# Performance work log

Measured on AMD Instinct MI355X. Metric: run time of the kernel, lower is better.

The kernel has to match this reference:

```python
import jax, jax.numpy as jnp
import numpy as np
from jax import lax

B, H, W, C, NH = 16, 56, 56, 192, 6
L = H * W
DH = C // NH            # 32
HID = 4 * C             # 768
ETA = 1.0 / DH          # TTT inner-loop learning rate
EPS = 1e-5

# ---- RoPE rotation tables (deterministic buffer, shape (H, W, C//2)) ----
_kmax = C // 4
_theta = 1.0 / (10000.0 ** (np.arange(_kmax) / _kmax))
_ii, _jj = np.meshgrid(np.arange(H), np.arange(W), indexing='ij')
_ang = np.concatenate([_ii[..., None] * _theta, _jj[..., None] * _theta], axis=-1)  # (H,W,C/2)
_COS = jnp.asarray(np.cos(_ang), dtype=jnp.float32)
_SIN = jnp.asarray(np.sin(_ang), dtype=jnp.float32)


def layernorm(x, g, b):
    mu = jnp.mean(x, axis=-1, keepdims=True)
    var = jnp.mean(jnp.square(x - mu), axis=-1, keepdims=True)
    return (x - mu) * lax.rsqrt(var + EPS) * g + b


def dwconv3x3(x_blc, w, b):
    # x: (B, L, Ch) -> depthwise 3x3 conv over (H, W) -> (B, L, Ch)
    Ch = x_blc.shape[-1]
    xi = x_blc.reshape(B, H, W, Ch).transpose(0, 3, 1, 2)  # NCHW
    y = lax.conv_general_dilated(xi, w, (1, 1), 'SAME', feature_group_count=Ch,
                                 dimension_numbers=('NCHW', 'OIHW', 'NCHW'))
    y = y + b[None, :, None, None]
    return y.transpose(0, 2, 3, 1).reshape(B, L, Ch)


def rope(x):
    # x: (B, L, C); rotate complex pairs with 2D axial angles
    xr = x.reshape(B, H, W, C // 2, 2)
    re, im = xr[..., 0], xr[..., 1]
    o_re = _COS * re - _SIN * im
    o_im = _SIN * re + _COS * im
    return jnp.stack([o_re, o_im], axis=-1).reshape(B, L, C)


def ttt_attn(xn, qkv_w, qkv_b, W0, proj_w, proj_b):
    qkv = xn @ qkv_w.T + qkv_b                      # (B, L, 3C)
    q, k, v = jnp.split(qkv, 3, axis=-1)
    q = rope(q) * (DH ** -0.5)
    k = rope(k)

    def to_heads(t):  # (B,L,C) -> (L, B*NH, DH)
        return t.reshape(B, L, NH, DH).transpose(1, 0, 2, 3).reshape(L, B * NH, DH)
    qs, ks, vs = to_heads(q), to_heads(k), to_heads(v)

    Wst0 = jnp.broadcast_to(W0[None], (B, NH, DH, DH)).reshape(B * NH, DH, DH)

    def step(Wst, qkv_t):
        qt, kt, vt = qkv_t
        pred = jnp.einsum('bij,bj->bi', Wst, kt)
        Wn = Wst - ETA * (pred - vt)[:, :, None] * kt[:, None, :]
        ot = jnp.einsum('bij,bj->bi', Wn, qt)
        return Wn, ot

    _, out = lax.scan(step, Wst0, (qs, ks, vs))     # out: (L, B*NH, DH)
    out = out.reshape(L, B, NH, DH).transpose(1, 0, 2, 3).reshape(B, L, C)
    return out @ proj_w.T + proj_b


def setup_inputs() -> dict:
    key = jax.random.key(0)
    ks = jax.random.split(key, 12)
    s = 0.02
    return {
        'x': jax.random.normal(ks[0], (B, L, C), jnp.float32),
        'cpe_w': jax.random.normal(ks[1], (C, 1, 3, 3), jnp.float32) * s,
        'cpe_b': jnp.zeros((C,), jnp.float32),
        'n1_g': jnp.ones((C,), jnp.float32),
        'n1_b': jnp.zeros((C,), jnp.float32),
        'qkv_w': jax.random.normal(ks[2], (3 * C, C), jnp.float32) * s,
        'qkv_b': jnp.zeros((3 * C,), jnp.float32),
        'W0': jax.random.normal(ks[3], (NH, DH, DH), jnp.float32) * s,
        'proj_w': jax.random.normal(ks[4], (C, C), jnp.float32) * s,
        'proj_b': jnp.zeros((C,), jnp.float32),
        'n2_g': jnp.ones((C,), jnp.float32),
        'n2_b': jnp.zeros((C,), jnp.float32),
        'fc1_w': jax.random.normal(ks[5], (HID, C), jnp.float32) * s,
        'fc1_b': jnp.zeros((HID,), jnp.float32),
        'dwc_w': jax.random.normal(ks[6], (HID, 1, 3, 3), jnp.float32) * s,
        'dwc_b': jnp.zeros((HID,), jnp.float32),
        'fc2_w': jax.random.normal(ks[7], (C, HID), jnp.float32) * s,
        'fc2_b': jnp.zeros((C,), jnp.float32),
    }


def reference(x, cpe_w, cpe_b, n1_g, n1_b, qkv_w, qkv_b, W0, proj_w, proj_b,
              n2_g, n2_b, fc1_w, fc1_b, dwc_w, dwc_b, fc2_w, fc2_b):
    # CPE: conditional positional encoding (depthwise conv residual)
    x = x + dwconv3x3(x, cpe_w, cpe_b)
    # TTT attention branch
    x = x + ttt_attn(layernorm(x, n1_g, n1_b), qkv_w, qkv_b, W0, proj_w, proj_b)
    # MLP branch with depthwise conv
    h1 = jax.nn.gelu(layernorm(x, n2_g, n2_b) @ fc1_w.T + fc1_b, approximate=False)
    h1 = jax.nn.gelu(h1 + dwconv3x3(h1, dwc_w, dwc_b), approximate=False)
    x = x + (h1 @ fc2_w.T + fc2_b)
    return x
```

## Files before the change

kernel.cpp:

```cpp
#include <hip/hip_runtime.h>
#include <hip/hip_bf16.h>

#define Bc 16
#define Hc 56
#define Wcc 56
#define Cc 192
#define NHc 6
#define Lc 3136
#define DHc 32
#define HIDc 768
#define NHEAD 96
#define Sc 32
#define NCHUNK 98
#define NPAIR (NHEAD*NCHUNK)
#define ROWS (Bc*Lc)
#define GR2 (ROWS/2)
#define ETAc (1.0f/32.0f)

typedef unsigned short u16;
typedef unsigned int u32;
typedef __attribute__((ext_vector_type(8))) short bf16x8;
typedef __attribute__((ext_vector_type(4))) float f32x4;
typedef __attribute__((ext_vector_type(16))) float f32x16;

__device__ __forceinline__ float b2f(u16 v){ u32 u = ((u32)v)<<16; float f; __builtin_memcpy(&f,&u,4); return f; }
__device__ __forceinline__ u16 f2b(float f){ u32 u; __builtin_memcpy(&u,&f,4); u32 r = u + 0x7FFFu + ((u>>16)&1u); return (u16)(r>>16); }
__device__ __forceinline__ f32x16 zero16(){ f32x16 z = {0,0,0,0,0,0,0,0,0,0,0,0,0,0,0,0}; return z; }

__device__ __forceinline__ void make_bfrags(const f32x16& t, int hi, bf16x8& b1, bf16x8& b2){
  u32 P[8], S[8];
  #pragma unroll
  for (int q=0;q<4;q++){
    #pragma unroll
    for (int j=0;j<2;j++){
      u32 r; float lo = t[4*q+2*j], hv = t[4*q+2*j+1];
      asm("v_cvt_pk_bf16_f32 %0, %1, %2" : "=v"(r) : "v"(lo), "v"(hv));
      P[2*q+j] = r;
    }
  }
  #pragma unroll
  for (int i=0;i<8;i++) S[i] = (u32)__shfl_xor((int)P[i], 32);
  union { u32 u[4]; bf16x8 v; } f1, f2;
  if (hi==0){ f1.u[0]=P[0]; f1.u[1]=P[1]; f1.u[2]=S[0]; f1.u[3]=S[1];
              f2.u[0]=P[4]; f2.u[1]=P[5]; f2.u[2]=S[4]; f2.u[3]=S[5]; }
  else      { f1.u[0]=S[2]; f1.u[1]=S[3]; f1.u[2]=P[2]; f1.u[3]=P[3];
              f2.u[0]=S[6]; f2.u[1]=S[7]; f2.u[2]=P[6]; f2.u[3]=P[7]; }
  b1 = f1.v; b2 = f2.v;
}

__global__ __launch_bounds__(256) void prep_kernel(
    const float* __restrict__ qkvw, const float* __restrict__ projw,
    const float* __restrict__ fc1w, const float* __restrict__ fc2w,
    const float* __restrict__ dwcw, const float* __restrict__ cpew,
    u16* __restrict__ wbqkv, u16* __restrict__ wbproj, u16* __restrict__ wbfc1,
    u16* __restrict__ wbfc2, float* __restrict__ dwt9, float* __restrict__ cwt9){
  int i = blockIdx.x*256 + threadIdx.x;
  if (i < 110592) wbqkv[i] = f2b(qkvw[i]);
  else if (i < 147456){ int j=i-110592; wbproj[j] = f2b(projw[j]); }
  else if (i < 294912){ int j=i-147456; wbfc1[j] = f2b(fc1w[j]); }
  else if (i < 442368){ int j=i-294912; wbfc2[j] = f2b(fc2w[j]); }
  else if (i < 449280){ int j=i-442368; int ch=j/9, t=j-ch*9; dwt9[t*HIDc+ch] = dwcw[j]; }
  else if (i < 451008){ int j=i-449280; int ch=j/9, t=j-ch*9; cwt9[t*Cc+ch] = cpew[j]; }
}

__global__ __launch_bounds__(256) void rope_tab_kernel(float* __restrict__ ct, float* __restrict__ st){
  int i = blockIdx.x*256 + threadIdx.x;
  int l = i/96, p = i - l*96;
  int h = l/Wcc, w = l - h*Wcc;
  int kk = (p<48)? p : p-48;
  float th = powf(10000.f, -(float)kk/48.f);
  float ang = (float)((p<48)? h : w) * th;
  ct[i] = cosf(ang);
  st[i] = sinf(ang);
}

__global__ __launch_bounds__(192) void cpe_ln_kernel(const float* __restrict__ x, const float* __restrict__ cwt9,
                                                     const float* __restrict__ bs, const float* __restrict__ g,
                                                     const float* __restrict__ b,
                                                     u16* __restrict__ x1, u16* __restrict__ xn){
  __shared__ float ps[192], pq[192], smu[8], srs[8];
  int tid = threadIdx.x;
  int rl = tid/24, sub = tid - rl*24, ch0 = sub*8;
  int row = blockIdx.x*8 + rl;
  int l = row % Lc; int h = l/Wcc, w = l - h*Wcc;
  const float* xp = x + (size_t)row*Cc + ch0;
  float acc[8];
  { f32x4 b0 = *(const f32x4*)(bs+ch0), b1v = *(const f32x4*)(bs+ch0+4);
    acc[0]=b0[0];acc[1]=b0[1];acc[2]=b0[2];acc[3]=b0[3];
    acc[4]=b1v[0];acc[5]=b1v[1];acc[6]=b1v[2];acc[7]=b1v[3]; }
  #pragma unroll
  for (int kh=0;kh<3;kh++){
    int hh = h+kh-1; if (hh<0 || hh>=Hc) continue;
    #pragma unroll
    for (int kw=0;kw<3;kw++){
      int ww = w+kw-1; if (ww<0 || ww>=Wcc) continue;
      const float* ip = xp + ((kh-1)*Wcc + (kw-1))*Cc;
      f32x4 i0 = *(const f32x4*)ip, i1 = *(const f32x4*)(ip+4);
      const float* wp = cwt9 + (kh*3+kw)*Cc + ch0;
      f32x4 w0 = *(const f32x4*)wp, w1 = *(const f32x4*)(wp+4);
      acc[0] += i0[0]*w0[0]; acc[1] += i0[1]*w0[1]; acc[2] += i0[2]*w0[2]; acc[3] += i0[3]*w0[3];
      acc[4] += i1[0]*w1[0]; acc[5] += i1[1]*w1[1]; acc[6] += i1[2]*w1[2]; acc[7] += i1[3]*w1[3];
    }
  }
  float val[8];
  { f32x4 c0 = *(const f32x4*)xp, c1 = *(const f32x4*)(xp+4);
    val[0]=c0[0]+acc[0]; val[1]=c0[1]+acc[1]; val[2]=c0[2]+acc[2]; val[3]=c0[3]+acc[3];
    val[4]=c1[0]+acc[4]; val[5]=c1[1]+acc[5]; val[6]=c1[2]+acc[6]; val[7]=c1[3]+acc[7]; }
  float s8=0.f, q8=0.f;
  #pragma unroll
  for (int j=0;j<8;j++){ s8 += val[j]; q8 += val[j]*val[j]; }
  ps[tid]=s8; pq[tid]=q8;
  __syncthreads();
  if (tid < 8){
    float s=0.f, q=0.f;
    #pragma unroll
    for (int k=0;k<24;k++){ s += ps[tid*24+k]; q += pq[tid*24+k]; }
    float mu = s*(1.f/Cc);
    float var = q*(1.f/Cc) - mu*mu;
    smu[tid] = mu; srs[tid] = rsqrtf(var + 1e-5f);
  }
  __syncthreads();
  float mu = smu[rl], rstd = srs[rl];
  union { bf16x8 v; u16 s[8]; } o1, o2;
  f32x4 g0 = *(const f32x4*)(g+ch0), g1 = *(const f32x4*)(g+ch0+4);
  f32x4 bb0 = *(const f32x4*)(b+ch0), bb1 = *(const f32x4*)(b+ch0+4);
  float gg[8] = {g0[0],g0[1],g0[2],g0[3],g1[0],g1[1],g1[2],g1[3]};
  float bbv[8] = {bb0[0],bb0[1],bb0[2],bb0[3],bb1[0],bb1[1],bb1[2],bb1[3]};
  #pragma unroll
  for (int j=0;j<8;j++){
    o1.s[j] = f2b(val[j]);
    o2.s[j] = f2b((val[j]-mu)*rstd*gg[j] + bbv[j]);
  }
  *(bf16x8*)(x1 + (size_t)row*Cc + ch0) = o1.v;
  *(bf16x8*)(xn + (size_t)row*Cc + ch0) = o2.v;
}

template<int MODE, int NB, int KT>
__global__ __launch_bounds__(256) void gemm_kernel(
    const u16* __restrict__ A, const u16* __restrict__ Wt,
    const float* __restrict__ bias,
    float* __restrict__ outf, u16* __restrict__ outb, u16* __restrict__ vdst,
    const u16* __restrict__ residb,
    const float* __restrict__ ct, const float* __restrict__ st,
    u16* __restrict__ q_s, u16* __restrict__ k_s,
    const float* __restrict__ lng, const float* __restrict__ lnb, u16* __restrict__ xnout)
{
  constexpr int NCH = KT/192;
  __shared__ __align__(16) u16 As[64*200];
  __shared__ __align__(16) u16 Osu[64*200];
  float* Os32 = (float*)Osu;
  int tid = threadIdx.x;
  int wid = tid>>6, lane = tid&63;
  int wr = wid>>1, wc = wid&1;
  int m0 = blockIdx.x*64;
  int ar = lane&15, kg = lane>>4;

  if constexpr (NCH == 1){
    #pragma unroll
    for (int j=0;j<6;j++){
      int g = j*256 + tid;
      int grow = g/24, gcol = (g - grow*24)*8;
      *(bf16x8*)(As + grow*200 + gcol) = *(const bf16x8*)(A + (size_t)(m0+grow)*192 + gcol);
    }
    __syncthreads();
    #pragma unroll
    for (int nb=0; nb<NB; nb++){
      const int nblk = nb*192;
      const int n0 = nblk + wc*96;
      f32x4 acc[2][6];
      #pragma unroll
      for (int f=0;f<2;f++)
        #pragma unroll
        for (int c=0;c<6;c++){ f32x4 z={0.f,0.f,0.f,0.f}; acc[f][c]=z; }
      bf16x8 bcur[6], bnxt[6];
      #pragma unroll
      for (int c=0;c<6;c++) bcur[c] = *(const bf16x8*)(Wt + (size_t)(n0 + c*16 + ar)*192 + kg*8);
      #pragma unroll
      for (int kc=0;kc<6;kc++){
        if (kc < 5){
          #pragma unroll
          for (int c=0;c<6;c++) bnxt[c] = *(const bf16x8*)(Wt + (size_t)(n0 + c*16 + ar)*192 + (kc+1)*32 + kg*8);
        }
        bf16x8 af[2];
        #pragma unroll
        for (int f=0;f<2;f++)
          af[f] = *(const bf16x8*)(As + (wr*32 + f*16 + ar)*200 + kc*32 + kg*8);
        #pragma unroll
        for (int f=0;f<2;f++)
          #pragma unroll
          for (int c=0;c<6;c++)
            acc[f][c] = __builtin_amdgcn_mfma_f32_16x16x32_bf16(af[f], bcur[c], acc[f][c], 0,0,0);
        #pragma unroll
        for (int c=0;c<6;c++) bcur[c] = bnxt[c];
      }
      __syncthreads();
      #pragma unroll
      for (int f=0;f<2;f++){
        #pragma unroll
        for (int c=0;c<6;c++){
          float bv = bias[n0 + c*16 + ar];
          #pragma unroll
          for (int j=0;j<4;j++){
            float v = acc[f][c][j] + bv;
            if (MODE==2) v = 0.5f*v*(1.f + erff(v*0.70710678118654752f));
            Osu[(wr*32 + f*16 + kg*4 + j)*200 + wc*96 + c*16 + ar] = f2b(v);
          }
        }
      }
      __syncthreads();
      #pragma unroll
      for (int j=0;j<6;j++){
        int g = j*256 + tid;
        int grow = g/24, gcol = (g - grow*24)*8;
        bf16x8 v = *(const bf16x8*)(Osu + grow*200 + gcol);
        int row = m0 + grow;
        if (MODE==2){
          *(bf16x8*)(outb + (size_t)row*HIDc + nblk + gcol) = v;
        } else if (MODE==1){
          bf16x8 rv = *(const bf16x8*)(residb + (size_t)row*Cc + gcol);
          union { bf16x8 v; u16 s[8]; } o;
          #pragma unroll
          for (int t=0;t<8;t++) o.s[t] = f2b(b2f((u16)v[t]) + b2f((u16)rv[t]));
          *(bf16x8*)(outb + (size_t)row*Cc + gcol) = o.v;
          *(bf16x8*)(Osu + grow*200 + gcol) = o.v;
        } else {
          int bb = row/Lc; int l = row - bb*Lc;
          int nh = gcol>>5, d = gcol&31;
          if (nb < 2){
            const bool isq = (nb == 0);
            int p0 = gcol>>1;
            f32x4 cv = *(const f32x4*)(ct + l*96 + p0);
            f32x4 sv = *(const f32x4*)(st + l*96 + p0);
            float sc = isq ? 0.1767766952966369f : 1.0f;
            union { bf16x8 v; u16 s[8]; } o;
            #pragma unroll
            for (int t=0;t<4;t++){
              float re = b2f((u16)v[2*t]), im = b2f((u16)v[2*t+1]);
              o.s[2*t]   = f2b((cv[t]*re - sv[t]*im)*sc);
              o.s[2*t+1] = f2b((sv[t]*re + cv[t]*im)*sc);
            }
            u16* dst = (isq ? q_s : k_s) + (((size_t)(bb*NHc+nh))*Lc + l)*DHc + d;
            *(bf16x8*)dst = o.v;
          } else {
            *(bf16x8*)(vdst + (((size_t)(bb*NHc+nh))*Lc + l)*DHc + d) = v;
          }
        }
      }
    }
    if (MODE==1){
      __syncthreads();
      int rowl = tid>>2, q = tid&3;
      const u16* orow = Osu + rowl*200 + q*48;
      float s=0.f, qq=0.f;
      #pragma unroll
      for (int c=0;c<48;c++){ float v = b2f(orow[c]); s += v; qq += v*v; }
      s += __shfl_xor(s,1); qq += __shfl_xor(qq,1);
      s += __shfl_xor(s,2); qq += __shfl_xor(qq,2);
      float mu = s*(1.f/192.f);
      float rstd = rsqrtf(qq*(1.f/192.f) - mu*mu + 1e-5f);
      int row = m0 + rowl;
      #pragma unroll
      for (int c8=0;c8<6;c8++){
        union { bf16x8 v; u16 s[8]; } ox;
        #pragma unroll
        for (int t=0;t<8;t++){
          int col = q*48 + c8*8 + t;
          ox.s[t] = f2b((b2f(orow[c8*8+t])-mu)*rstd*lng[col] + lnb[col]);
        }
        *(bf16x8*)(xnout + (size_t)row*Cc + q*48 + c8*8) = ox.v;
      }
    }
  } else {
    const int n0 = wc*96;
    f32x4 acc[2][6];
    #pragma unroll
    for (int f=0;f<2;f++)
      #pragma unroll
      for (int c=0;c<6;c++){ f32x4 z={0.f,0.f,0.f,0.f}; acc[f][c]=z; }
    bf16x8 bcur[6], bnxt[6];
    #pragma unroll
    for (int c=0;c<6;c++) bcur[c] = *(const bf16x8*)(Wt + (size_t)(n0 + c*16 + ar)*KT + kg*8);
    #pragma unroll
    for (int ch=0; ch<NCH; ch++){
      if (ch>0) __syncthreads();
      #pragma unroll
      for (int j=0;j<6;j++){
        int g = j*256 + tid;
        int grow = g/24, gcol = (g - grow*24)*8;
        *(bf16x8*)(As + grow*200 + gcol) = *(const bf16x8*)(A + (size_t)(m0+grow)*KT + ch*192 + gcol);
      }
      __syncthreads();
      #pragma unroll
      for (int kc=0;kc<6;kc++){
        int s = ch*6 + kc;
        if (s+1 < NCH*6){
          int koff = ((s+1)/6)*192 + ((s+1)%6)*32 + kg*8;
          #pragma unroll
          for (int c=0;c<6;c++) bnxt[c] = *(const bf16x8*)(Wt + (size_t)(n0 + c*16 + ar)*KT + koff);
        }
        bf16x8 af[2];
        #pragma unroll
        for (int f=0;f<2;f++)
          af[f] = *(const bf16x8*)(As + (wr*32 + f*16 + ar)*200 + kc*32 + kg*8);
        #pragma unroll
        for (int f=0;f<2;f++)
          #pragma unroll
          for (int c=0;c<6;c++)
            acc[f][c] = __builtin_amdgcn_mfma_f32_16x16x32_bf16(af[f], bcur[c], acc[f][c], 0,0,0);
        #pragma unroll
        for (int c=0;c<6;c++) bcur[c] = bnxt[c];
      }
    }
    #pragma unroll
    for (int half=0; half<2; half++){
      __syncthreads();
      if (wc==half){
        #pragma unroll
        for (int f=0;f<2;f++){
          #pragma unroll
          for (int c=0;c<6;c++){
            float bv = bias[n0 + c*16 + ar];
            #pragma unroll
            for (int j=0;j<4;j++)
              Os32[(wr*32 + f*16 + kg*4 + j)*100 + c*16 + ar] = acc[f][c][j] + bv;
          }
        }
      }
      __syncthreads();
      #pragma unroll
      for (int j=0;j<6;j++){
        int g = j*256 + tid;
        int grow = g/24, qcol = (g - grow*24)*4;
        f32x4 v = *(const f32x4*)(Os32 + grow*100 + qcol);
        int row = m0 + grow, colg = half*96 + qcol;
        const u16* rp = residb + (size_t)row*Cc + colg;
        v[0] += b2f(rp[0]); v[1] += b2f(rp[1]); v[2] += b2f(rp[2]); v[3] += b2f(rp[3]);
        *(f32x4*)(outf + (size_t)row*Cc + colg) = v;
      }
    }
  }
}

__global__ __launch_bounds__(256) void dwc_kernel(const u16* __restrict__ h1, const float* __restrict__ wt9,
                                                  const float* __restrict__ bs, u16* __restrict__ h2, int row0){
  int gid = blockIdx.x*256 + threadIdx.x;
  int cg = gid % 96; int lrow = gid / 96; int ch0 = cg*8;
  int row = row0 + lrow;
  int l = row % Lc; int h = l/Wcc, w = l - h*Wcc;
  const u16* hp = h1 + (size_t)lrow*HIDc + ch0;
  float acc[8];
  { f32x4 b0 = *(const f32x4*)(bs+ch0), b1v = *(const f32x4*)(bs+ch0+4);
    acc[0]=b0[0];acc[1]=b0[1];acc[2]=b0[2];acc[3]=b0[3];
    acc[4]=b1v[0];acc[5]=b1v[1];acc[6]=b1v[2];acc[7]=b1v[3]; }
  #pragma unroll
  for (int kh=0;kh<3;kh++){
    int hh = h+kh-1; if (hh<0 || hh>=Hc) continue;
    #pragma unroll
    for (int kw=0;kw<3;kw++){
      int ww = w+kw-1; if (ww<0 || ww>=Wcc) continue;
      bf16x8 iv = *(const bf16x8*)(hp + ((kh-1)*Wcc + (kw-1))*HIDc);
      const float* wp = wt9 + (kh*3+kw)*HIDc + ch0;
      f32x4 w0 = *(const f32x4*)wp, w1 = *(const f32x4*)(wp+4);
      acc[0] += b2f((u16)iv[0])*w0[0]; acc[1] += b2f((u16)iv[1])*w0[1];
      acc[2] += b2f((u16)iv[2])*w0[2]; acc[3] += b2f((u16)iv[3])*w0[3];
      acc[4] += b2f((u16)iv[4])*w1[0]; acc[5] += b2f((u16)iv[5])*w1[1];
      acc[6] += b2f((u16)iv[6])*w1[2]; acc[7] += b2f((u16)iv[7])*w1[3];
    }
  }
  bf16x8 cv = *(const bf16x8*)hp;
  union { bf16x8 v; u16 s[8]; } ov;
  #pragma unroll
  for (int j=0;j<8;j++){
    float v = b2f((u16)cv[j]) + acc[j];
    ov.s[j] = f2b(0.5f*v*(1.f + erff(v*0.70710678118654752f)));
  }
  *(bf16x8*)(h2 + (size_t)lrow*HIDc + ch0) = ov.v;
}

__global__ __launch_bounds__(64) void ttta_kernel(const u16* __restrict__ k_s, const u16* __restrict__ v_s,
                                                  u16* __restrict__ af_s, u16* __restrict__ bc_s){
  __shared__ float Gl[1024];
  __shared__ u16 LK[32*40];
  __shared__ float LU[32*33];
  __shared__ float LR[32*33];
  int pair = blockIdx.x;
  int head = pair / NCHUNK;
  int l0 = (pair - head*NCHUNK) * Sc;
  int lane = threadIdx.x; int rr = lane&31; int hi = lane>>5; int ks = hi*8;
  const u16* kb = k_s + ((size_t)head*Lc + l0)*DHc;
  bf16x8 a0 = *(const bf16x8*)(kb + rr*32 + ks);
  bf16x8 a1 = *(const bf16x8*)(kb + rr*32 + 16 + ks);
  *(bf16x8*)(LK + rr*40 + ks) = a0;
  *(bf16x8*)(LK + rr*40 + 16 + ks) = a1;
  f32x16 g = zero16();
  g = __builtin_amdgcn_mfma_f32_32x32x16_bf16(a0, a0, g, 0,0,0);
  g = __builtin_amdgcn_mfma_f32_32x32x16_bf16(a1, a1, g, 0,0,0);
  #pragma unroll
  for (int reg=0;reg<16;reg++){
    int i = (reg&3) + 8*(reg>>2) + 4*hi;
    Gl[i*32 + rr] = ETAc * g[reg];
  }
  __syncthreads();
  float X[32];
  if (lane < 32){
    #pragma unroll
    for (int i=0;i<32;i++) X[i] = ETAc * b2f(v_s[((size_t)head*Lc + l0 + i)*DHc + lane]);
  } else {
    int m = lane-32;
    #pragma unroll
    for (int i=0;i<32;i++) X[i] = ETAc * b2f(kb[i*32 + m]);
  }
  #pragma unroll
  for (int i=1;i<32;i++){
    float a = X[i];
    #pragma unroll
    for (int j=0;j<i;j++) a -= Gl[i*32+j]*X[j];
    X[i] = a;
  }
  if (lane < 32){
    #pragma unroll
    for (int i=0;i<32;i++) LU[lane*33 + i] = X[i];
  } else {
    #pragma unroll
    for (int i=0;i<32;i++) LR[(lane&31)*33 + i] = X[i];
  }
  __syncthreads();
  union { bf16x8 v; u16 s[8]; } kc1, kc2, uc1, uc2, rc1, rc2;
  #pragma unroll
  for (int s=0;s<8;s++){
    kc1.s[s] = LK[(ks+s)*40 + rr];
    kc2.s[s] = LK[(16+ks+s)*40 + rr];
    uc1.s[s] = f2b(LU[rr*33 + ks+s]);
    uc2.s[s] = f2b(LU[rr*33 + 16+ks+s]);
    rc1.s[s] = f2b(LR[rr*33 + ks+s]);
    rc2.s[s] = f2b(LR[rr*33 + 16+ks+s]);
  }
  f32x16 bacc = zero16();
  bacc = __builtin_amdgcn_mfma_f32_32x32x16_bf16(kc1.v, uc1.v, bacc, 0,0,0);
  bacc = __builtin_amdgcn_mfma_f32_32x32x16_bf16(kc2.v, uc2.v, bacc, 0,0,0);
  union { bf16x8 v; u16 s[8]; } bo1, bo2;
  #pragma unroll
  for (int r=0;r<8;r++){ bo1.s[r] = f2b(bacc[r]); bo2.s[r] = f2b(bacc[8+r]); }
  *(bf16x8*)(bc_s + (size_t)pair*1024 + lane*16) = bo1.v;
  *(bf16x8*)(bc_s + (size_t)pair*1024 + lane*16 + 8) = bo2.v;
  f32x16 aacc = zero16();
  aacc = __builtin_amdgcn_mfma_f32_32x32x16_bf16(rc1.v, kc1.v, aacc, 0,0,0);
  aacc = __builtin_amdgcn_mfma_f32_32x32x16_bf16(rc2.v, kc2.v, aacc, 0,0,0);
  f32x16 an;
  #pragma unroll
  for (int r=0;r<16;r++) an[r] = -aacc[r];
  bf16x8 f1, f2;
  make_bfrags(an, hi, f1, f2);
  *(bf16x8*)(af_s + (size_t)pair*1024 + lane*16) = f1;
  *(bf16x8*)(af_s + (size_t)pair*1024 + lane*16 + 8) = f2;
}

__global__ __launch_bounds__(64) void tttb_kernel(const u16* __restrict__ af_s, const u16* __restrict__ bc_s,
                                                  const float* __restrict__ W0, u16* __restrict__ w_snap){
  int head = blockIdx.x; int nh = head % NHc;
  int lane = threadIdx.x; int rr = lane&31; int hi = lane>>5;
  f32x16 T;
  const float* w0r = W0 + nh*1024 + rr*32 + 4*hi;
  #pragma unroll
  for (int q=0;q<4;q++){
    f32x4 v = *(const f32x4*)(w0r + 8*q);
    T[4*q+0]=v[0]; T[4*q+1]=v[1]; T[4*q+2]=v[2]; T[4*q+3]=v[3];
  }
  size_t hb = (size_t)head*NCHUNK;
  const bf16x8* afp = (const bf16x8*)(af_s + hb*1024);
  const bf16x8* bcp = (const bf16x8*)(bc_s + hb*1024);
  bf16x8 A1 = afp[lane*2], A2 = afp[lane*2+1];
  bf16x8 Bv1 = bcp[lane*2], Bv2 = bcp[lane*2+1];
  bf16x8 b1, b2;
  make_bfrags(T, hi, b1, b2);
  for (int c=0;c<NCHUNK;c++){
    bf16x8 nA1=A1, nA2=A2, nB1=Bv1, nB2=Bv2;
    if (c+1 < NCHUNK){
      int base = (c+1)*128 + lane*2;
      nA1 = afp[base]; nA2 = afp[base+1];
      nB1 = bcp[base]; nB2 = bcp[base+1];
    }
    u16* wrow = w_snap + (hb + c)*1024 + rr*32;
    *(bf16x8*)(wrow + hi*8) = b1;
    *(bf16x8*)(wrow + 16 + hi*8) = b2;
    f32x16 acc;
    #pragma unroll
    for (int r=0;r<8;r++){ acc[r] = T[r] + b2f((u16)Bv1[r]); acc[8+r] = T[8+r] + b2f((u16)Bv2[r]); }
    acc = __builtin_amdgcn_mfma_f32_32x32x16_bf16(A1, b1, acc, 0,0,0);
    acc = __builtin_amdgcn_mfma_f32_32x32x16_bf16(A2, b2, acc, 0,0,0);
    T = acc;
    make_bfrags(T, hi, b1, b2);
    A1=nA1; A2=nA2; Bv1=nB1; Bv2=nB2;
  }
}

__global__ __launch_bounds__(64) void tttc_kernel(const u16* __restrict__ q_s, const u16* __restrict__ k_s,
                                                  const u16* __restrict__ v_s, const u16* __restrict__ w_snap,
                                                  u16* __restrict__ o_bf){
  __shared__ float Gl[1024];
  __shared__ float LU[32*33];
  __shared__ float LR[32*33];
  __shared__ __align__(16) u16 Pl[32*40];
  int pair = blockIdx.x;
  int head = pair / NCHUNK;
  int ch = pair - head*NCHUNK;
  int l0 = ch*Sc;
  int lane = threadIdx.x; int rr = lane&31; int hi = lane>>5; int ks = hi*8;
  const u16* kb = k_s + ((size_t)head*Lc + l0)*DHc;
  const u16* qb = q_s + ((size_t)head*Lc + l0)*DHc;
  bf16x8 k0 = *(const bf16x8*)(kb + rr*32 + ks);
  bf16x8 k1 = *(const bf16x8*)(kb + rr*32 + 16 + ks);
  f32x16 g = zero16();
  g = __builtin_amdgcn_mfma_f32_32x32x16_bf16(k0, k0, g, 0,0,0);
  g = __builtin_amdgcn_mfma_f32_32x32x16_bf16(k1, k1, g, 0,0,0);
  #pragma unroll
  for (int reg=0;reg<16;reg++){
    int i = (reg&3) + 8*(reg>>2) + 4*hi;
    Gl[i*32 + rr] = ETAc * g[reg];
  }
  __syncthreads();
  float X[32];
  if (lane < 32){
    #pragma unroll
    for (int i=0;i<32;i++) X[i] = ETAc * b2f(v_s[((size_t)head*Lc + l0 + i)*DHc + lane]);
  } else {
    int m = lane-32;
    #pragma unroll
    for (int i=0;i<32;i++) X[i] = ETAc * b2f(kb[i*32 + m]);
  }
  #pragma unroll
  for (int i=1;i<32;i++){
    float a = X[i];
    #pragma unroll
    for (int j=0;j<i;j++) a -= Gl[i*32+j]*X[j];
    X[i] = a;
  }
  if (lane < 32){
    #pragma unroll
    for (int i=0;i<32;i++) LU[lane*33 + i] = X[i];
  } else {
    #pragma unroll
    for (int i=0;i<32;i++) LR[(lane&31)*33 + i] = X[i];
  }
  __syncthreads();
  bf16x8 q0 = *(const bf16x8*)(qb + rr*32 + ks);
  bf16x8 q1 = *(const bf16x8*)(qb + rr*32 + 16 + ks);
  f32x16 p = zero16();
  p = __builtin_amdgcn_mfma_f32_32x32x16_bf16(q0, k0, p, 0,0,0);
  p = __builtin_amdgcn_mfma_f32_32x32x16_bf16(q1, k1, p, 0,0,0);
  #pragma unroll
  for (int reg=0;reg<16;reg++){
    int i = (reg&3)+8*(reg>>2)+4*hi;
    Pl[i*40+rr] = (rr<=i) ? f2b(p[reg]) : (u16)0;
  }
  const u16* wsb = w_snap + (size_t)pair*1024;
  bf16x8 tb0 = *(const bf16x8*)(wsb + rr*32 + ks);
  bf16x8 tb1 = *(const bf16x8*)(wsb + rr*32 + 16 + ks);
  f32x16 wr;
  #pragma unroll
  for (int r=0;r<16;r++){
    int i = (r&3)+8*(r>>2)+4*hi;
    wr[r] = LU[rr*33 + i];
  }
  union { bf16x8 v; u16 s[8]; } rn0, rn1;
  #pragma unroll
  for (int s=0;s<8;s++){
    rn0.s[s] = f2b(-LR[(ks+s)*33 + rr]);
    rn1.s[s] = f2b(-LR[(16+ks+s)*33 + rr]);
  }
  wr = __builtin_amdgcn_mfma_f32_32x32x16_bf16(rn0.v, tb0, wr, 0,0,0);
  wr = __builtin_amdgcn_mfma_f32_32x32x16_bf16(rn1.v, tb1, wr, 0,0,0);
  bf16x8 wb0, wb1;
  make_bfrags(wr, hi, wb0, wb1);
  __syncthreads();
  f32x16 o = zero16();
  o = __builtin_amdgcn_mfma_f32_32x32x16_bf16(q0, tb0, o, 0,0,0);
  o = __builtin_amdgcn_mfma_f32_32x32x16_bf16(q1, tb1, o, 0,0,0);
  bf16x8 pa0 = *(const bf16x8*)(Pl + rr*40 + ks);
  bf16x8 pa1 = *(const bf16x8*)(Pl + rr*40 + 16 + ks);
  o = __builtin_amdgcn_mfma_f32_32x32x16_bf16(pa0, wb0, o, 0,0,0);
  o = __builtin_amdgcn_mfma_f32_32x32x16_bf16(pa1, wb1, o, 0,0,0);
  int bb = head/NHc, nh = head - bb*NHc;
  #pragma unroll
  for (int reg=0;reg<16;reg++){
    int i = (reg&3)+8*(reg>>2)+4*hi;
    o_bf[((size_t)(bb*Lc + l0 + i))*Cc + nh*32 + rr] = f2b(o[reg]);
  }
}

extern "C" void kernel_launch(void* const* d_in, const int* in_sizes, int n_in,
                              void* d_out, int out_size, void* d_ws, size_t ws_size,
                              hipStream_t stream){
  const float* x     = (const float*)d_in[0];
  const float* cpe_w = (const float*)d_in[1];
  const float* cpe_b = (const float*)d_in[2];
  const float* n1_g  = (const float*)d_in[3];
  const float* n1_b  = (const float*)d_in[4];
  const float* qkv_w = (const float*)d_in[5];
  const float* qkv_b = (const float*)d_in[6];
  const float* W0    = (const float*)d_in[7];
  const float* proj_w= (const float*)d_in[8];
  const float* proj_b= (const float*)d_in[9];
  const float* n2_g  = (const float*)d_in[10];
  const float* n2_b  = (const float*)d_in[11];
  const float* fc1_w = (const float*)d_in[12];
  const float* fc1_b = (const float*)d_in[13];
  const float* dwc_w = (const float*)d_in[14];
  const float* dwc_b = (const float*)d_in[15];
  const float* fc2_w = (const float*)d_in[16];
  const float* fc2_b = (const float*)d_in[17];

  char* ws = (char*)d_ws;
  size_t off = 0;
  auto alloc = [&](size_t bytes)->char*{
    char* p = ws + off;
    off += (bytes + 255) & ~(size_t)255;
    return p;
  };
  u16* wbqkv = (u16*)alloc((size_t)576*192*2);
  u16* wbproj= (u16*)alloc((size_t)192*192*2);
  u16* wbfc1 = (u16*)alloc((size_t)768*192*2);
  u16* wbfc2 = (u16*)alloc((size_t)192*768*2);
  float* dwt9 = (float*)alloc((size_t)9*HIDc*4);
  float* cwt9 = (float*)alloc((size_t)9*Cc*4);
  float* ctab = (float*)alloc((size_t)Lc*96*4);
  float* stab = (float*)alloc((size_t)Lc*96*4);
  u16* regA = (u16*)alloc((size_t)ROWS*Cc*2);
  u16* regB = (u16*)alloc((size_t)ROWS*Cc*2);
  u16* regC = (u16*)alloc((size_t)NHEAD*Lc*DHc*2);
  u16* regD = (u16*)alloc((size_t)NHEAD*Lc*DHc*2);
  u16* regE = (u16*)alloc((size_t)NHEAD*Lc*DHc*2);
  u16* regF = (u16*)alloc((size_t)NPAIR*1024*2);
  u16* af_s = (u16*)alloc((size_t)NPAIR*1024*2);
  u16* bc = (u16*)d_out;

  u16* x1 = regA;
  u16* x2b = regA;
  u16* xn = regB;
  u16* obf = regB;
  u16* xn2 = regB;
  u16* qs = regC;
  u16* vs = regD;
  u16* ksb = regE;
  u16* wsn = regF;
  u16* h1 = regD;
  u16* h2 = regF;

  prep_kernel<<<(451008+255)/256,256,0,stream>>>(qkv_w, proj_w, fc1_w, fc2_w, dwc_w, cpe_w,
                                                 wbqkv, wbproj, wbfc1, wbfc2, dwt9, cwt9);
  rope_tab_kernel<<<(Lc*96)/256,256,0,stream>>>(ctab, stab);

  cpe_ln_kernel<<<ROWS/8,192,0,stream>>>(x, cwt9, cpe_b, n1_g, n1_b, x1, xn);
  gemm_kernel<0,3,192><<<ROWS/64,256,0,stream>>>(xn, wbqkv, qkv_b,
      nullptr, nullptr, vs, nullptr, ctab, stab, qs, ksb, nullptr, nullptr, nullptr);
  ttta_kernel<<<NPAIR,64,0,stream>>>(ksb, vs, af_s, bc);
  tttb_kernel<<<NHEAD,64,0,stream>>>(af_s, bc, W0, wsn);
  tttc_kernel<<<NPAIR,64,0,stream>>>(qs, ksb, vs, wsn, obf);
  gemm_kernel<1,1,192><<<ROWS/64,256,0,stream>>>(obf, wbproj, proj_b,
      nullptr, x2b, nullptr, x1, nullptr, nullptr, nullptr, nullptr, n2_g, n2_b, xn2);
  for (int g4=0; g4<2; g4++){
    const u16* a_in = xn2 + (size_t)g4*GR2*Cc;
    float* xo = (float*)d_out + (size_t)g4*GR2*Cc;
    const u16* res = x2b + (size_t)g4*GR2*Cc;
    gemm_kernel<2,4,192><<<GR2/64,256,0,stream>>>(a_in, wbfc1, fc1_b,
        nullptr, h1, nullptr, nullptr, nullptr, nullptr, nullptr, nullptr, nullptr, nullptr, nullptr);
    dwc_kernel<<<(GR2*96)/256,256,0,stream>>>(h1, dwt9, dwc_b, h2, g4*GR2);
    gemm_kernel<3,1,768><<<GR2/64,256,0,stream>>>(h2, wbfc2, fc2_b,
        xo, nullptr, nullptr, res, nullptr, nullptr, nullptr, nullptr, nullptr, nullptr, nullptr);
  }
}
```

Baseline: 520.2 us.

## Double TTT chunk size to 64 to halve the sequential inter-chunk scan

Changes the chunked TTT formulation from 32-token to 64-token chunks, so the serial per-head scan kernel (tttb) runs 49 steps instead of 98. The intra-chunk triangular solve grows to 64x64, the Gram and causal-score blocks become 2x2 tiles of 32x32 MFMAs, and the intermediate solve results are stored in LDS as bf16. This targets the latency-bound serial recurrence that runs on only 96 single-wavefront blocks. In exchange the per-chunk solve does about four times the serial FMA work with 64 registers of X per lane, which raises register pressure, and the extra bf16 rounding of intermediates may change numerics.

```diff
diff --git a/kernel.cpp b/kernel.cpp
--- a/kernel.cpp
+++ b/kernel.cpp
@@ -10,9 +10,8 @@
 #define DHc 32
 #define HIDc 768
 #define NHEAD 96
-#define Sc 32
-#define NCHUNK 98
-#define NPAIR (NHEAD*NCHUNK)
+#define NCH2 49
+#define NPAIR2 (NHEAD*NCH2)
 #define ROWS (Bc*Lc)
 #define GR2 (ROWS/2)
 #define ETAc (1.0f/32.0f)
@@ -377,75 +376,93 @@
   *(bf16x8*)(h2 + (size_t)lrow*HIDc + ch0) = ov.v;
 }
 
+__device__ __forceinline__ void solve64(const u16* kb, const u16* vb, int lane, int rr, int hi, int ks,
+                                        float* Gl, u16* LU, u16* LR,
+                                        bf16x8& kA0, bf16x8& kA1, bf16x8& kB0, bf16x8& kB1){
+  kA0 = *(const bf16x8*)(kb + rr*32 + ks);
+  kA1 = *(const bf16x8*)(kb + rr*32 + 16 + ks);
+  kB0 = *(const bf16x8*)(kb + (32+rr)*32 + ks);
+  kB1 = *(const bf16x8*)(kb + (32+rr)*32 + 16 + ks);
+  f32x16 g00 = zero16(), g10 = zero16(), g11 = zero16();
+  g00 = __builtin_amdgcn_mfma_f32_32x32x16_bf16(kA0, kA0, g00, 0,0,0);
+  g00 = __builtin_amdgcn_mfma_f32_32x32x16_bf16(kA1, kA1, g00, 0,0,0);
+  g10 = __builtin_amdgcn_mfma_f32_32x32x16_bf16(kB0, kA0, g10, 0,0,0);
+  g10 = __builtin_amdgcn_mfma_f32_32x32x16_bf16(kB1, kA1, g10, 0,0,0);
+  g11 = __builtin_amdgcn_mfma_f32_32x32x16_bf16(kB0, kB0, g11, 0,0,0);
+  g11 = __builtin_amdgcn_mfma_f32_32x32x16_bf16(kB1, kB1, g11, 0,0,0);
+  #pragma unroll
+  for (int reg=0;reg<16;reg++){
+    int i = (reg&3) + 8*(reg>>2) + 4*hi;
+    Gl[i*64 + rr]          = ETAc * g00[reg];
+    Gl[(32+i)*64 + rr]     = ETAc * g10[reg];
+    Gl[(32+i)*64 + 32+rr]  = ETAc * g11[reg];
+  }
+  __syncthreads();
+  float X[64];
+  if (lane < 32){
+    #pragma unroll
+    for (int i=0;i<64;i++) X[i] = ETAc * b2f(vb[i*32 + lane]);
+  } else {
+    int m = lane-32;
+    #pragma unroll
+    for (int i=0;i<64;i++) X[i] = ETAc * b2f(kb[i*32 + m]);
+  }
+  #pragma unroll
+  for (int i=1;i<64;i++){
+    float a = X[i];
+    #pragma unroll
+    for (int j=0;j<i;j++) a -= Gl[i*64+j]*X[j];
+    X[i] = a;
+  }
+  u16* Lx = (lane<32 ? LU : LR) + (lane&31)*72;
+  #pragma unroll
+  for (int i=0;i<64;i++) Lx[i] = f2b(X[i]);
+  __syncthreads();
+}
+
 __global__ __launch_bounds__(64) void ttta_kernel(const u16* __restrict__ k_s, const u16* __restrict__ v_s,
                                                   u16* __restrict__ af_s, u16* __restrict__ bc_s){
-  __shared__ float Gl[1024];
-  __shared__ u16 LK[32*40];
-  __shared__ float LU[32*33];
-  __shared__ float LR[32*33];
+  __shared__ float Gl[64*64];
+  __shared__ __align__(16) u16 LK[64*40];
+  __shared__ u16 LU[32*72];
+  __shared__ u16 LR[32*72];
   int pair = blockIdx.x;
-  int head = pair / NCHUNK;
-  int l0 = (pair - head*NCHUNK) * Sc;
+  int head = pair / NCH2;
+  int l0 = (pair - head*NCH2) * 64;
   int lane = threadIdx.x; int rr = lane&31; int hi = lane>>5; int ks = hi*8;
   const u16* kb = k_s + ((size_t)head*Lc + l0)*DHc;
-  bf16x8 a0 = *(const bf16x8*)(kb + rr*32 + ks);
-  bf16x8 a1 = *(const bf16x8*)(kb + rr*32 + 16 + ks);
-  *(bf16x8*)(LK + rr*40 + ks) = a0;
-  *(bf16x8*)(LK + rr*40 + 16 + ks) = a1;
-  f32x16 g = zero16();
-  g = __builtin_amdgcn_mfma_f32_32x32x16_bf16(a0, a0, g, 0,0,0);
-  g = __builtin_amdgcn_mfma_f32_32x32x16_bf16(a1, a1, g, 0,0,0);
-  #pragma unroll
-  for (int reg=0;reg<16;reg++){
-    int i = (reg&3) + 8*(reg>>2) + 4*hi;
-    Gl[i*32 + rr] = ETAc * g[reg];
-  }
-  __syncthreads();
-  float X[32];
-  if (lane < 32){
-    #pragma unroll
-    for (int i=0;i<32;i++) X[i] = ETAc * b2f(v_s[((size_t)head*Lc + l0 + i)*DHc + lane]);
-  } else {
-    int m = lane-32;
-    #pragma unroll
-    for (int i=0;i<32;i++) X[i] = ETAc * b2f(kb[i*32 + m]);
-  }
-  #pragma unroll
-  for (int i=1;i<32;i++){
-    float a = X[i];
-    #pragma unroll
-    for (int j=0;j<i;j++) a -= Gl[i*32+j]*X[j];
-    X[i] = a;
-  }
-  if (lane < 32){
-    #pragma unroll
-    for (int i=0;i<32;i++) LU[lane*33 + i] = X[i];
-  } else {
-    #pragma unroll
-    for (int i=0;i<32;i++) LR[(lane&31)*33 + i] = X[i];
-  }
-  __syncthreads();
-  union { bf16x8 v; u16 s[8]; } kc1, kc2, uc1, uc2, rc1, rc2;
-  #pragma unroll
-  for (int s=0;s<8;s++){
-    kc1.s[s] = LK[(ks+s)*40 + rr];
-    kc2.s[s] = LK[(16+ks+s)*40 + rr];
-    uc1.s[s] = f2b(LU[rr*33 + ks+s]);
-    uc2.s[s] = f2b(LU[rr*33 + 16+ks+s]);
-    rc1.s[s] = f2b(LR[rr*33 + ks+s]);
-    rc2.s[s] = f2b(LR[rr*33 + 16+ks+s]);
+  const u16* vb = v_s + ((size_t)head*Lc + l0)*DHc;
+  bf16x8 kA0,kA1,kB0,kB1;
+  {
+    bf16x8 a = *(const bf16x8*)(kb + rr*32 + ks);
+    bf16x8 b = *(const bf16x8*)(kb + rr*32 + 16 + ks);
+    bf16x8 c = *(const bf16x8*)(kb + (32+rr)*32 + ks);
+    bf16x8 d = *(const bf16x8*)(kb + (32+rr)*32 + 16 + ks);
+    *(bf16x8*)(LK + rr*40 + ks) = a;      *(bf16x8*)(LK + rr*40 + 16 + ks) = b;
+    *(bf16x8*)(LK + (32+rr)*40 + ks) = c; *(bf16x8*)(LK + (32+rr)*40 + 16 + ks) = d;
+  }
+  solve64(kb, vb, lane, rr, hi, ks, Gl, LU, LR, kA0, kA1, kB0, kB1);
+  union { bf16x8 v; u16 s[8]; } kc[4], uc[4], rc[4];
+  #pragma unroll
+  for (int t=0;t<4;t++){
+    #pragma unroll
+    for (int s=0;s<8;s++){
+      kc[t].s[s] = LK[(16*t + ks + s)*40 + rr];
+      uc[t].s[s] = LU[rr*72 + 16*t + ks + s];
+      rc[t].s[s] = LR[rr*72 + 16*t + ks + s];
+    }
   }
   f32x16 bacc = zero16();
-  bacc = __builtin_amdgcn_mfma_f32_32x32x16_bf16(kc1.v, uc1.v, bacc, 0,0,0);
-  bacc = __builtin_amdgcn_mfma_f32_32x32x16_bf16(kc2.v, uc2.v, bacc, 0,0,0);
+  #pragma unroll
+  for (int t=0;t<4;t++) bacc = __builtin_amdgcn_mfma_f32_32x32x16_bf16(kc[t].v, uc[t].v, bacc, 0,0,0);
   union { bf16x8 v; u16 s[8]; } bo1, bo2;
   #pragma unroll
   for (int r=0;r<8;r++){ bo1.s[r] = f2b(bacc[r]); bo2.s[r] = f2b(bacc[8+r]); }
   *(bf16x8*)(bc_s + (size_t)pair*1024 + lane*16) = bo1.v;
   *(bf16x8*)(bc_s + (size_t)pair*1024 + lane*16 + 8) = bo2.v;
   f32x16 aacc = zero16();
-  aacc = __builtin_amdgcn_mfma_f32_32x32x16_bf16(rc1.v, kc1.v, aacc, 0,0,0);
-  aacc = __builtin_amdgcn_mfma_f32_32x32x16_bf16(rc2.v, kc2.v, aacc, 0,0,0);
+  #pragma unroll
+  for (int t=0;t<4;t++) aacc = __builtin_amdgcn_mfma_f32_32x32x16_bf16(rc[t].v, kc[t].v, aacc, 0,0,0);
   f32x16 an;
   #pragma unroll
   for (int r=0;r<16;r++) an[r] = -aacc[r];
@@ -466,16 +483,16 @@
     f32x4 v = *(const f32x4*)(w0r + 8*q);
     T[4*q+0]=v[0]; T[4*q+1]=v[1]; T[4*q+2]=v[2]; T[4*q+3]=v[3];
   }
-  size_t hb = (size_t)head*NCHUNK;
+  size_t hb = (size_t)head*NCH2;
   const bf16x8* afp = (const bf16x8*)(af_s + hb*1024);
   const bf16x8* bcp = (const bf16x8*)(bc_s + hb*1024);
   bf16x8 A1 = afp[lane*2], A2 = afp[lane*2+1];
   bf16x8 Bv1 = bcp[lane*2], Bv2 = bcp[lane*2+1];
   bf16x8 b1, b2;
   make_bfrags(T, hi, b1, b2);
-  for (int c=0;c<NCHUNK;c++){
+  for (int c=0;c<NCH2;c++){
     bf16x8 nA1=A1, nA2=A2, nB1=Bv1, nB2=Bv2;
-    if (c+1 < NCHUNK){
+    if (c+1 < NCH2){
       int base = (c+1)*128 + lane*2;
       nA1 = afp[base]; nA2 = afp[base+1];
       nB1 = bcp[base]; nB2 = bcp[base+1];
@@ -497,94 +514,112 @@
 __global__ __launch_bounds__(64) void tttc_kernel(const u16* __restrict__ q_s, const u16* __restrict__ k_s,
                                                   const u16* __restrict__ v_s, const u16* __restrict__ w_snap,
                                                   u16* __restrict__ o_bf){
-  __shared__ float Gl[1024];
-  __shared__ float LU[32*33];
-  __shared__ float LR[32*33];
-  __shared__ __align__(16) u16 Pl[32*40];
+  __shared__ float Gl[64*64];
+  __shared__ u16 LU[32*72];
+  __shared__ u16 LR[32*72];
+  __shared__ __align__(16) u16 Pl[64*72];
   int pair = blockIdx.x;
-  int head = pair / NCHUNK;
-  int ch = pair - head*NCHUNK;
-  int l0 = ch*Sc;
+  int head = pair / NCH2;
+  int l0 = (pair - head*NCH2) * 64;
   int lane = threadIdx.x; int rr = lane&31; int hi = lane>>5; int ks = hi*8;
   const u16* kb = k_s + ((size_t)head*Lc + l0)*DHc;
+  const u16* vb = v_s + ((size_t)head*Lc + l0)*DHc;
   const u16* qb = q_s + ((size_t)head*Lc + l0)*DHc;
-  bf16x8 k0 = *(const bf16x8*)(kb + rr*32 + ks);
-  bf16x8 k1 = *(const bf16x8*)(kb + rr*32 + 16 + ks);
-  f32x16 g = zero16();
-  g = __builtin_amdgcn_mfma_f32_32x32x16_bf16(k0, k0, g, 0,0,0);
-  g = __builtin_amdgcn_mfma_f32_32x32x16_bf16(k1, k1, g, 0,0,0);
-  #pragma unroll
-  for (int reg=0;reg<16;reg++){
-    int i = (reg&3) + 8*(reg>>2) + 4*hi;
-    Gl[i*32 + rr] = ETAc * g[reg];
-  }
-  __syncthreads();
-  float X[32];
-  if (lane < 32){
-    #pragma unroll
-    for (int i=0;i<32;i++) X[i] = ETAc * b2f(v_s[((size_t)head*Lc + l0 + i)*DHc + lane]);
-  } else {
-    int m = lane-32;
-    #pragma unroll
-    for (int i=0;i<32;i++) X[i] = ETAc * b2f(kb[i*32 + m]);
-  }
-  #pragma unroll
-  for (int i=1;i<32;i++){
-    float a = X[i];
-    #pragma unroll
-    for (int j=0;j<i;j++) a -= Gl[i*32+j]*X[j];
-    X[i] = a;
-  }
-  if (lane < 32){
-    #pragma unroll
-    for (int i=0;i<32;i++) LU[lane*33 + i] = X[i];
-  } else {
-    #pragma unroll
-    for (int i=0;i<32;i++) LR[(lane&31)*33 + i] = X[i];
-  }
-  __syncthreads();
-  bf16x8 q0 = *(const bf16x8*)(qb + rr*32 + ks);
-  bf16x8 q1 = *(const bf16x8*)(qb + rr*32 + 16 + ks);
-  f32x16 p = zero16();
-  p = __builtin_amdgcn_mfma_f32_32x32x16_bf16(q0, k0, p, 0,0,0);
-  p = __builtin_amdgcn_mfma_f32_32x32x16_bf16(q1, k1, p, 0,0,0);
-  #pragma unroll
-  for (int reg=0;reg<16;reg++){
-    int i = (reg&3)+8*(reg>>2)+4*hi;
-    Pl[i*40+rr] = (rr<=i) ? f2b(p[reg]) : (u16)0;
+  bf16x8 kA0,kA1,kB0,kB1;
+  solve64(kb, vb, lane, rr, hi, ks, Gl, LU, LR, kA0, kA1, kB0, kB1);
+  bf16x8 qA0 = *(const bf16x8*)(qb + rr*32 + ks);
+  bf16x8 qA1 = *(const bf16x8*)(qb + rr*32 + 16 + ks);
+  bf16x8 qB0 = *(const bf16x8*)(qb + (32+rr)*32 + ks);
+  bf16x8 qB1 = *(const bf16x8*)(qb + (32+rr)*32 + 16 + ks);
+  {
+    f32x16 p = zero16();
+    p = __builtin_amdgcn_mfma_f32_32x32x16_bf16(qA0, kA0, p, 0,0,0);
+    p = __builtin_amdgcn_mfma_f32_32x32x16_bf16(qA1, kA1, p, 0,0,0);
+    #pragma unroll
+    for (int reg=0;reg<16;reg++){
+      int i = (reg&3)+8*(reg>>2)+4*hi;
+      Pl[i*72 + rr] = (rr<=i) ? f2b(p[reg]) : (u16)0;
+      Pl[i*72 + 32 + rr] = (u16)0;
+    }
+  }
+  {
+    f32x16 p = zero16();
+    p = __builtin_amdgcn_mfma_f32_32x32x16_bf16(qB0, kA0, p, 0,0,0);
+    p = __builtin_amdgcn_mfma_f32_32x32x16_bf16(qB1, kA1, p, 0,0,0);
+    #pragma unroll
+    for (int reg=0;reg<16;reg++){
+      int i = (reg&3)+8*(reg>>2)+4*hi;
+      Pl[(32+i)*72 + rr] = f2b(p[reg]);
+    }
+  }
+  {
+    f32x16 p = zero16();
+    p = __builtin_amdgcn_mfma_f32_32x32x16_bf16(qB0, kB0, p, 0,0,0);
+    p = __builtin_amdgcn_mfma_f32_32x32x16_bf16(qB1, kB1, p, 0,0,0);
+    #pragma unroll
+    for (int reg=0;reg<16;reg++){
+      int i = (reg&3)+8*(reg>>2)+4*hi;
+      Pl[(32+i)*72 + 32 + rr] = (rr<=i) ? f2b(p[reg]) : (u16)0;
+    }
   }
   const u16* wsb = w_snap + (size_t)pair*1024;
   bf16x8 tb0 = *(const bf16x8*)(wsb + rr*32 + ks);
   bf16x8 tb1 = *(const bf16x8*)(wsb + rr*32 + 16 + ks);
-  f32x16 wr;
+  f32x16 wrA, wrB;
   #pragma unroll
   for (int r=0;r<16;r++){
     int i = (r&3)+8*(r>>2)+4*hi;
-    wr[r] = LU[rr*33 + i];
-  }
-  union { bf16x8 v; u16 s[8]; } rn0, rn1;
+    wrA[r] = b2f(LU[rr*72 + i]);
+    wrB[r] = b2f(LU[rr*72 + 32 + i]);
+  }
+  union { bf16x8 v; u16 s[8]; } rnA0, rnA1, rnB0, rnB1;
   #pragma unroll
   for (int s=0;s<8;s++){
-    rn0.s[s] = f2b(-LR[(ks+s)*33 + rr]);
-    rn1.s[s] = f2b(-LR[(16+ks+s)*33 + rr]);
-  }
-  wr = __builtin_amdgcn_mfma_f32_32x32x16_bf16(rn0.v, tb0, wr, 0,0,0);
-  wr = __builtin_amdgcn_mfma_f32_32x32x16_bf16(rn1.v, tb1, wr, 0,0,0);
-  bf16x8 wb0, wb1;
-  make_bfrags(wr, hi, wb0, wb1);
+    rnA0.s[s] = LR[(ks+s)*72 + rr] ^ (u16)0x8000;
+    rnA1.s[s] = LR[(16+ks+s)*72 + rr] ^ (u16)0x8000;
+    rnB0.s[s] = LR[(ks+s)*72 + 32 + rr] ^ (u16)0x8000;
+    rnB1.s[s] = LR[(16+ks+s)*72 + 32 + rr] ^ (u16)0x8000;
+  }
+  wrA = __builtin_amdgcn_mfma_f32_32x32x16_bf16(rnA0.v, tb0, wrA, 0,0,0);
+  wrA = __builtin_amdgcn_mfma_f32_32x32x16_bf16(rnA1.v, tb1, wrA, 0,0,0);
+  wrB = __builtin_amdgcn_mfma_f32_32x32x16_bf16(rnB0.v, tb0, wrB, 0,0,0);
+  wrB = __builtin_amdgcn_mfma_f32_32x32x16_bf16(rnB1.v, tb1, wrB, 0,0,0);
+  bf16x8 wbA0, wbA1, wbB0, wbB1;
+  make_bfrags(wrA, hi, wbA0, wbA1);
+  make_bfrags(wrB, hi, wbB0, wbB1);
   __syncthreads();
-  f32x16 o = zero16();
-  o = __builtin_amdgcn_mfma_f32_32x32x16_bf16(q0, tb0, o, 0,0,0);
-  o = __builtin_amdgcn_mfma_f32_32x32x16_bf16(q1, tb1, o, 0,0,0);
-  bf16x8 pa0 = *(const bf16x8*)(Pl + rr*40 + ks);
-  bf16x8 pa1 = *(const bf16x8*)(Pl + rr*40 + 16 + ks);
-  o = __builtin_amdgcn_mfma_f32_32x32x16_bf16(pa0, wb0, o, 0,0,0);
-  o = __builtin_amdgcn_mfma_f32_32x32x16_bf16(pa1, wb1, o, 0,0,0);
   int bb = head/NHc, nh = head - bb*NHc;
-  #pragma unroll
-  for (int reg=0;reg<16;reg++){
-    int i = (reg&3)+8*(reg>>2)+4*hi;
-    o_bf[((size_t)(bb*Lc + l0 + i))*Cc + nh*32 + rr] = f2b(o[reg]);
+  {
+    f32x16 o = zero16();
+    o = __builtin_amdgcn_mfma_f32_32x32x16_bf16(qA0, tb0, o, 0,0,0);
+    o = __builtin_amdgcn_mfma_f32_32x32x16_bf16(qA1, tb1, o, 0,0,0);
+    bf16x8 pa0 = *(const bf16x8*)(Pl + rr*72 + ks);
+    bf16x8 pa1 = *(const bf16x8*)(Pl + rr*72 + 16 + ks);
+    o = __builtin_amdgcn_mfma_f32_32x32x16_bf16(pa0, wbA0, o, 0,0,0);
+    o = __builtin_amdgcn_mfma_f32_32x32x16_bf16(pa1, wbA1, o, 0,0,0);
+    #pragma unroll
+    for (int reg=0;reg<16;reg++){
+      int i = (reg&3)+8*(reg>>2)+4*hi;
+      o_bf[((size_t)(bb*Lc + l0 + i))*Cc + nh*32 + rr] = f2b(o[reg]);
+    }
+  }
+  {
+    f32x16 o = zero16();
+    o = __builtin_amdgcn_mfma_f32_32x32x16_bf16(qB0, tb0, o, 0,0,0);
+    o = __builtin_amdgcn_mfma_f32_32x32x16_bf16(qB1, tb1, o, 0,0,0);
+    bf16x8 pb0 = *(const bf16x8*)(Pl + (32+rr)*72 + ks);
+    bf16x8 pb1 = *(const bf16x8*)(Pl + (32+rr)*72 + 16 + ks);
+    bf16x8 pb2 = *(const bf16x8*)(Pl + (32+rr)*72 + 32 + ks);
+    bf16x8 pb3 = *(const bf16x8*)(Pl + (32+rr)*72 + 48 + ks);
+    o = __builtin_amdgcn_mfma_f32_32x32x16_bf16(pb0, wbA0, o, 0,0,0);
+    o = __builtin_amdgcn_mfma_f32_32x32x16_bf16(pb1, wbA1, o, 0,0,0);
+    o = __builtin_amdgcn_mfma_f32_32x32x16_bf16(pb2, wbB0, o, 0,0,0);
+    o = __builtin_amdgcn_mfma_f32_32x32x16_bf16(pb3, wbB1, o, 0,0,0);
+    #pragma unroll
+    for (int reg=0;reg<16;reg++){
+      int i = (reg&3)+8*(reg>>2)+4*hi;
+      o_bf[((size_t)(bb*Lc + l0 + 32 + i))*Cc + nh*32 + rr] = f2b(o[reg]);
+    }
   }
 }
 
@@ -630,8 +665,8 @@
   u16* regC = (u16*)alloc((size_t)NHEAD*Lc*DHc*2);
   u16* regD = (u16*)alloc((size_t)NHEAD*Lc*DHc*2);
   u16* regE = (u16*)alloc((size_t)NHEAD*Lc*DHc*2);
-  u16* regF = (u16*)alloc((size_t)NPAIR*1024*2);
-  u16* af_s = (u16*)alloc((size_t)NPAIR*1024*2);
+  u16* regF = (u16*)alloc((size_t)NHEAD*Lc*DHc*2);
+  u16* af_s = (u16*)alloc((size_t)NHEAD*Lc*DHc*2);
   u16* bc = (u16*)d_out;
 
   u16* x1 = regA;
@@ -653,9 +688,9 @@
   cpe_ln_kernel<<<ROWS/8,192,0,stream>>>(x, cwt9, cpe_b, n1_g, n1_b, x1, xn);
   gemm_kernel<0,3,192><<<ROWS/64,256,0,stream>>>(xn, wbqkv, qkv_b,
       nullptr, nullptr, vs, nullptr, ctab, stab, qs, ksb, nullptr, nullptr, nullptr);
-  ttta_kernel<<<NPAIR,64,0,stream>>>(ksb, vs, af_s, bc);
+  ttta_kernel<<<NPAIR2,64,0,stream>>>(ksb, vs, af_s, bc);
   tttb_kernel<<<NHEAD,64,0,stream>>>(af_s, bc, W0, wsn);
-  tttc_kernel<<<NPAIR,64,0,stream>>>(qs, ksb, vs, wsn, obf);
+  tttc_kernel<<<NPAIR2,64,0,stream>>>(qs, ksb, vs, wsn, obf);
   gemm_kernel<1,1,192><<<ROWS/64,256,0,stream>>>(obf, wbproj, proj_b,
       nullptr, x2b, nullptr, x1, nullptr, nullptr, nullptr, nullptr, n2_g, n2_b, xn2);
   for (int g4=0; g4<2; g4++){
```

New measurement: 564.5 us. +8.5%, slower.
